# Performance work log

Hardware: AMD Instinct MI355X
Metric: run time of the kernel (lower is better)

## Reference

```python
import jax, jax.numpy as jnp
import numpy as np

B, N, D_IN, D, H_HEADS, DH, M_LAND, ITERS, NCLS = 2, 16384, 1024, 512, 8, 64, 256, 6, 2


def layer_norm(x, g, b, eps=1e-5):
    mu = x.mean(-1, keepdims=True)
    var = ((x - mu) ** 2).mean(-1, keepdims=True)
    return (x - mu) * jax.lax.rsqrt(var + eps) * g + b


def pinv_iter(x, iters):
    # Moore-Penrose pseudo-inverse via Newton-Schulz style iteration (lucidrains nystrom-attention)
    col = jnp.abs(x).sum(-1)
    row = jnp.abs(x).sum(-2)
    z = jnp.swapaxes(x, -1, -2) / (jnp.max(col) * jnp.max(row))
    I = jnp.eye(x.shape[-1], dtype=x.dtype)
    for _ in range(iters):
        xz = x @ z
        z = 0.25 * z @ (13.0 * I - xz @ (15.0 * I - xz @ (7.0 * I - xz)))
    return z


def depthwise_conv(x, w, pad_h, pad_w):
    # x: [B,C,H,W], w: [C,1,kh,kw], groups=C
    return jax.lax.conv_general_dilated(
        x, w, (1, 1), ((pad_h, pad_h), (pad_w, pad_w)),
        dimension_numbers=('NCHW', 'OIHW', 'NCHW'), feature_group_count=x.shape[1])


def nystrom_attention(x, w_qkv, w_out, b_out, res_w):
    b, n, _ = x.shape
    pad = (-n) % M_LAND
    xp = jnp.pad(x, ((0, 0), (pad, 0), (0, 0)))  # pad at front
    npad = n + pad
    qkv = xp @ w_qkv                              # [b, npad, 3D]
    q, k, v = jnp.split(qkv, 3, axis=-1)
    split_heads = lambda t: t.reshape(b, npad, H_HEADS, DH).transpose(0, 2, 1, 3)
    q = split_heads(q) * (DH ** -0.5)
    k = split_heads(k)
    v = split_heads(v)
    l = npad // M_LAND
    # landmarks: mean over contiguous groups '(m l) d -> m d'
    ql = q.reshape(b, H_HEADS, M_LAND, l, DH).mean(3)
    kl = k.reshape(b, H_HEADS, M_LAND, l, DH).mean(3)
    sim1 = jnp.einsum('bhnd,bhmd->bhnm', q, kl)   # [b,h,npad,m]
    sim2 = jnp.einsum('bhid,bhjd->bhij', ql, kl)  # [b,h,m,m]
    sim3 = jnp.einsum('bhmd,bhnd->bhmn', ql, k)   # [b,h,m,npad]
    a1 = jax.nn.softmax(sim1, -1)
    a2 = jax.nn.softmax(sim2, -1)
    a3 = jax.nn.softmax(sim3, -1)
    a2inv = pinv_iter(a2, ITERS)
    out = (a1 @ a2inv) @ (a3 @ v)                 # [b,h,npad,dh]
    # residual depthwise conv over sequence dim, kernel (33,1), per head
    out = out + depthwise_conv(v, res_w, 16, 0)
    out = out.transpose(0, 2, 1, 3).reshape(b, npad, D)
    out = out @ w_out + b_out                     # dropout is identity in eval
    return out[:, -n:]


def ppeg(x, Hs, Ws, w7, b7, w5, b5, w3, b3):
    Bx, _, C = x.shape
    cls_tok, feat = x[:, :1], x[:, 1:]
    f = feat.transpose(0, 2, 1).reshape(Bx, C, Hs, Ws)
    y = (f
         + depthwise_conv(f, w7, 3, 3) + b7[None, :, None, None]
         + depthwise_conv(f, w5, 2, 2) + b5[None, :, None, None]
         + depthwise_conv(f, w3, 1, 1) + b3[None, :, None, None])
    y = y.reshape(Bx, C, Hs * Ws).transpose(0, 2, 1)
    return jnp.concatenate([cls_tok, y], axis=1)


def _forward(x, w_feat, b_feat, cls_token, ln1_g, ln1_b, qkv1, out1_w, out1_b, res1_w,
             ppeg_w7, ppeg_b7, ppeg_w5, ppeg_b5, ppeg_w3, ppeg_b3,
             ln2_g, ln2_b, qkv2, out2_w, out2_b, res2_w, lnf_g, lnf_b, cls_w, cls_b):
    h = jax.nn.gelu(x @ w_feat + b_feat)          # feature embed (dropout off)
    n = h.shape[1]
    side = int(np.ceil(np.sqrt(n)))
    add = side * side - n
    h = jnp.concatenate([h, h[:, :add]], axis=1)  # pad bag to square
    cls = jnp.broadcast_to(cls_token, (h.shape[0], 1, D))
    h = jnp.concatenate([cls, h], axis=1)
    h = h + nystrom_attention(layer_norm(h, ln1_g, ln1_b), qkv1, out1_w, out1_b, res1_w)
    h = ppeg(h, side, side, ppeg_w7, ppeg_b7, ppeg_w5, ppeg_b5, ppeg_w3, ppeg_b3)
    h = h + nystrom_attention(layer_norm(h, ln2_g, ln2_b), qkv2, out2_w, out2_b, res2_w)
    feat0 = layer_norm(h, lnf_g, lnf_b)[:, 0]
    return feat0 @ cls_w + cls_b                  # logits [B, n_classes]


def setup_inputs() -> dict:
    key = jax.random.key(0)
    ks = jax.random.split(key, 16)
    s = jnp.float32(0.02)
    return {
        'x': jax.random.normal(ks[0], (B, N, D_IN), jnp.float32),
        'w_feat': jax.random.normal(ks[1], (D_IN, D), jnp.float32) * s,
        'b_feat': jnp.zeros((D,), jnp.float32),
        'cls_token': jax.random.normal(ks[2], (1, 1, D), jnp.float32) * jnp.float32(1e-6),
        'ln1_g': jnp.ones((D,), jnp.float32), 'ln1_b': jnp.zeros((D,), jnp.float32),
        'qkv1': jax.random.normal(ks[3], (D, 3 * D), jnp.float32) * s,
        'out1_w': jax.random.normal(ks[4], (D, D), jnp.float32) * s,
        'out1_b': jnp.zeros((D,), jnp.float32),
        'res1_w': jax.random.normal(ks[5], (H_HEADS, 1, 33, 1), jnp.float32) * s,
        'ppeg_w7': jax.random.normal(ks[6], (D, 1, 7, 7), jnp.float32) * s,
        'ppeg_b7': jnp.zeros((D,), jnp.float32),
        'ppeg_w5': jax.random.normal(ks[7], (D, 1, 5, 5), jnp.float32) * s,
        'ppeg_b5': jnp.zeros((D,), jnp.float32),
        'ppeg_w3': jax.random.normal(ks[8], (D, 1, 3, 3), jnp.float32) * s,
        'ppeg_b3': jnp.zeros((D,), jnp.float32),
        'ln2_g': jnp.ones((D,), jnp.float32), 'ln2_b': jnp.zeros((D,), jnp.float32),
        'qkv2': jax.random.normal(ks[9], (D, 3 * D), jnp.float32) * s,
        'out2_w': jax.random.normal(ks[10], (D, D), jnp.float32) * s,
        'out2_b': jnp.zeros((D,), jnp.float32),
        'res2_w': jax.random.normal(ks[11], (H_HEADS, 1, 33, 1), jnp.float32) * s,
        'lnf_g': jnp.ones((D,), jnp.float32), 'lnf_b': jnp.zeros((D,), jnp.float32),
        'cls_w': jax.random.normal(ks[12], (D, NCLS), jnp.float32) * s,
        'cls_b': jnp.zeros((NCLS,), jnp.float32),
    }


def reference(x, w_feat, b_feat, cls_token, ln1_g, ln1_b, qkv1, out1_w, out1_b, res1_w,
              ppeg_w7, ppeg_b7, ppeg_w5, ppeg_b5, ppeg_w3, ppeg_b3,
              ln2_g, ln2_b, qkv2, out2_w, out2_b, res2_w, lnf_g, lnf_b, cls_w, cls_b):
    return _forward(x, w_feat, b_feat, cls_token, ln1_g, ln1_b, qkv1, out1_w, out1_b, res1_w,
                    ppeg_w7, ppeg_b7, ppeg_w5, ppeg_b5, ppeg_w3, ppeg_b3,
                    ln2_g, ln2_b, qkv2, out2_w, out2_b, res2_w, lnf_g, lnf_b, cls_w, cls_b)
```

## Files before the change

kernel.cpp:

```cpp
#include <hip/hip_runtime.h>
#include <cstdint>
#include <cstddef>

#define BB 2
#define TT 16385
#define NPAD 16640
#define DD 512
#define HH 8
#define DHH 64
#define MLAND 256
#define PADF 255
#define A3KC 26
#define A3CH 640

typedef __attribute__((ext_vector_type(8))) _Float16 f16x8;
typedef __attribute__((ext_vector_type(4))) float f32x4;

__device__ __forceinline__ float gelu_f(float v) {
  float c = 0.7978845608028654f * (v + 0.044715f * v * v * v);
  return 0.5f * v * (1.0f + tanhf(c));
}

__device__ __forceinline__ unsigned short f16_1(float a) {
  _Float16 h = (_Float16)a;
  return __builtin_bit_cast(unsigned short, h);
}
__device__ __forceinline__ float f16f(unsigned u) {
  return (float)__builtin_bit_cast(_Float16, (unsigned short)(u & 0xffffu));
}
__device__ __forceinline__ unsigned pk_f16(float a, float b) {
  return (unsigned)f16_1(a) | ((unsigned)f16_1(b) << 16);
}
__device__ __forceinline__ void split2h(float a, float b, unsigned& hi, unsigned& lo) {
  _Float16 ah = (_Float16)a, bh = (_Float16)b;
  hi = (unsigned)__builtin_bit_cast(unsigned short, ah) |
       ((unsigned)__builtin_bit_cast(unsigned short, bh) << 16);
  lo = pk_f16(a - (float)ah, b - (float)bh);
}
__device__ __forceinline__ void store4h(float4 v, unsigned short* dh,
                                        unsigned short* dl) {
  unsigned h0, l0, h1, l1;
  split2h(v.x, v.y, h0, l0);
  split2h(v.z, v.w, h1, l1);
  *(uint2*)dh = make_uint2(h0, h1);
  *(uint2*)dl = make_uint2(l0, l1);
}

__global__ void k_set_cls(float* __restrict__ h, const float* __restrict__ cls) {
  h[(size_t)blockIdx.x * TT * DD + threadIdx.x] = cls[threadIdx.x];
}
__global__ void k_copy_cls(float* __restrict__ dst, const float* __restrict__ src) {
  size_t o = (size_t)blockIdx.x * TT * DD + threadIdx.x;
  dst[o] = src[o];
}

__global__ __launch_bounds__(256) void k_cvt_wt(
    const float* __restrict__ W, unsigned short* __restrict__ Wth, int K, int N) {
  __shared__ float tile[32][33];
  int kb = blockIdx.x * 32, nb = blockIdx.y * 32;
  int t = threadIdx.x;
  int tr = t >> 3, tc4 = (t & 7) * 4;
  float4 v = *(const float4*)(W + (size_t)(kb + tr) * N + nb + tc4);
  tile[tr][tc4 + 0] = v.x;
  tile[tr][tc4 + 1] = v.y;
  tile[tr][tc4 + 2] = v.z;
  tile[tr][tc4 + 3] = v.w;
  __syncthreads();
  int n = nb + tr;
  ushort4 hs;
  hs.x = f16_1(tile[tc4 + 0][tr]);
  hs.y = f16_1(tile[tc4 + 1][tr]);
  hs.z = f16_1(tile[tc4 + 2][tr]);
  hs.w = f16_1(tile[tc4 + 3][tr]);
  *(ushort4*)(Wth + (size_t)n * K + kb + tc4) = hs;
}

template <int MODE>
__global__ __launch_bounds__(512) void k_gemm_mfma(
    const float* __restrict__ A, const unsigned short* __restrict__ Aph,
    const unsigned short* __restrict__ Apl, const unsigned short* __restrict__ Wth,
    const float* __restrict__ bias, void* __restrict__ Cv, int M, int K, int N,
    int lda) {
  __shared__ short Ash[128][44];
  __shared__ short Asl[128][44];
  __shared__ short Bsh[256][44];
  const int t = threadIdx.x;
  int nRow = gridDim.x, nCol = gridDim.y;
  int lin = blockIdx.x + blockIdx.y * nRow;
  int chunk = 8 * nCol;
  int group = lin / chunk;
  int rem = lin - group * chunk;
  int gbase = group * 8;
  int Geff = nRow - gbase;
  if (Geff > 8) Geff = 8;
  const int rb = (gbase + rem % Geff) * 128;
  const int cb = (rem / Geff) * 256;
  const float* Ab = A;
  float* Cf = (float*)Cv;
  unsigned short* Ch = (unsigned short*)Cv;
  if (MODE == 2) {
    int b = blockIdx.z;
    Ab = A + (size_t)b * NPAD * DD + (size_t)PADF * DD;
    Cf = (float*)Cv + (size_t)b * TT * DD;
  }
  const int lane = t & 63, wv = t >> 6;
  const int wr = wv >> 2, wc = wv & 3;
  const int fr = lane & 15, kg = lane >> 4;
  const int srow = t >> 2, skh = (t & 3) * 8;
  const int brow = t >> 1, bkh = (t & 1) * 16;

  f32x4 acc[4][4];
  f32x4 zero4 = {0.f, 0.f, 0.f, 0.f};
#pragma unroll
  for (int i = 0; i < 4; ++i)
#pragma unroll
    for (int j = 0; j < 4; ++j) acc[i][j] = zero4;

  for (int k0 = 0; k0 < K; k0 += 32) {
    __syncthreads();
    if (MODE == 1) {
      const unsigned short* ph = Aph + (size_t)(rb + srow) * lda + k0 + skh;
      const unsigned short* pl = Apl + (size_t)(rb + srow) * lda + k0 + skh;
      *(uint4*)&Ash[srow][skh] = *(const uint4*)ph;
      *(uint4*)&Asl[srow][skh] = *(const uint4*)pl;
    } else {
      int grow = rb + srow;
      float4 f0 = {0, 0, 0, 0}, f1 = {0, 0, 0, 0};
      if (grow < M) {
        const float* p = Ab + (size_t)grow * lda + k0 + skh;
        f0 = *(const float4*)p;
        f1 = *(const float4*)(p + 4);
      }
      unsigned h0, h1, h2, h3, l0, l1, l2, l3;
      split2h(f0.x, f0.y, h0, l0);
      split2h(f0.z, f0.w, h1, l1);
      split2h(f1.x, f1.y, h2, l2);
      split2h(f1.z, f1.w, h3, l3);
      *(uint4*)&Ash[srow][skh] = make_uint4(h0, h1, h2, h3);
      *(uint4*)&Asl[srow][skh] = make_uint4(l0, l1, l2, l3);
    }
    {
      const unsigned short* ph = Wth + (size_t)(cb + brow) * K + k0 + bkh;
      *(uint4*)&Bsh[brow][bkh] = *(const uint4*)ph;
      *(uint4*)&Bsh[brow][bkh + 8] = *(const uint4*)(ph + 8);
    }
    __syncthreads();
    f16x8 ah[4], al[4];
#pragma unroll
    for (int mf = 0; mf < 4; ++mf) {
      ah[mf] = *(const f16x8*)&Ash[wr * 64 + mf * 16 + fr][kg * 8];
      al[mf] = *(const f16x8*)&Asl[wr * 64 + mf * 16 + fr][kg * 8];
    }
#pragma unroll
    for (int nf = 0; nf < 4; ++nf) {
      f16x8 bhf = *(const f16x8*)&Bsh[wc * 64 + nf * 16 + fr][kg * 8];
#pragma unroll
      for (int mf = 0; mf < 4; ++mf) {
        acc[mf][nf] =
            __builtin_amdgcn_mfma_f32_16x16x32_f16(ah[mf], bhf, acc[mf][nf], 0, 0, 0);
        acc[mf][nf] =
            __builtin_amdgcn_mfma_f32_16x16x32_f16(al[mf], bhf, acc[mf][nf], 0, 0, 0);
      }
    }
  }
#pragma unroll
  for (int mf = 0; mf < 4; ++mf) {
#pragma unroll
    for (int r = 0; r < 4; ++r) {
      int row = rb + wr * 64 + mf * 16 + kg * 4 + r;
      if (MODE == 2 && row >= M) continue;
      size_t orow = (MODE == 0) ? (size_t)(row + (row >> 14) + 1) : (size_t)row;
#pragma unroll
      for (int nf = 0; nf < 4; ++nf) {
        int col = cb + wc * 64 + nf * 16 + fr;
        float v = acc[mf][nf][r];
        if (MODE == 0) {
          Cf[orow * DD + col] = gelu_f(v + bias[col]);
        } else if (MODE == 1) {
          Ch[orow * (size_t)N + col] = f16_1(v);
        } else {
          float old = Cf[orow * DD + col];
          Cf[orow * DD + col] = old + v + bias[col];
        }
      }
    }
  }
}

__global__ __launch_bounds__(256) void k_ln_pad(
    unsigned short* __restrict__ xph, unsigned short* __restrict__ xpl,
    const float* __restrict__ h, const float* __restrict__ gam,
    const float* __restrict__ bet) {
  int w = threadIdx.x >> 6, lane = threadIdx.x & 63;
  int row = blockIdx.x * 4 + w;
  if (row >= BB * TT) return;
  int b = row / TT, i = row - b * TT;
  const float* src = h + (size_t)row * DD;
  float4 x0 = *(const float4*)(src + lane * 4);
  float4 x1 = *(const float4*)(src + 256 + lane * 4);
  float s = x0.x + x0.y + x0.z + x0.w + x1.x + x1.y + x1.z + x1.w;
  for (int o = 32; o; o >>= 1) s += __shfl_xor(s, o);
  float mu = s * (1.f / 512.f);
  float q = (x0.x - mu) * (x0.x - mu) + (x0.y - mu) * (x0.y - mu) +
            (x0.z - mu) * (x0.z - mu) + (x0.w - mu) * (x0.w - mu) +
            (x1.x - mu) * (x1.x - mu) + (x1.y - mu) * (x1.y - mu) +
            (x1.z - mu) * (x1.z - mu) + (x1.w - mu) * (x1.w - mu);
  for (int o = 32; o; o >>= 1) q += __shfl_xor(q, o);
  float rs = rsqrtf(q * (1.f / 512.f) + 1e-5f);
  float4 g0 = *(const float4*)(gam + lane * 4);
  float4 g1 = *(const float4*)(gam + 256 + lane * 4);
  float4 b0 = *(const float4*)(bet + lane * 4);
  float4 b1 = *(const float4*)(bet + 256 + lane * 4);
  float4 o0, o1;
  o0.x = (x0.x - mu) * rs * g0.x + b0.x;
  o0.y = (x0.y - mu) * rs * g0.y + b0.y;
  o0.z = (x0.z - mu) * rs * g0.z + b0.z;
  o0.w = (x0.w - mu) * rs * g0.w + b0.w;
  o1.x = (x1.x - mu) * rs * g1.x + b1.x;
  o1.y = (x1.y - mu) * rs * g1.y + b1.y;
  o1.z = (x1.z - mu) * rs * g1.z + b1.z;
  o1.w = (x1.w - mu) * rs * g1.w + b1.w;
  size_t ro = ((size_t)b * NPAD + PADF + i) * DD;
  store4h(o0, xph + ro + lane * 4, xpl + ro + lane * 4);
  store4h(o1, xph + ro + 256 + lane * 4, xpl + ro + 256 + lane * 4);
}

__global__ void k_zero_pad(unsigned short* __restrict__ xph,
                           unsigned short* __restrict__ xpl) {
  int r = blockIdx.x;
  int b = r / PADF, j = r - b * PADF;
  size_t ro = ((size_t)b * NPAD + j) * DD;
  ((unsigned*)(xph + ro))[threadIdx.x] = 0u;
  ((unsigned*)(xpl + ro))[threadIdx.x] = 0u;
}

__global__ __launch_bounds__(256) void k_landmarks(
    float* __restrict__ ql, float* __restrict__ kl,
    const unsigned short* __restrict__ qkv) {
  int t = threadIdx.x;
  int mi = t >> 6, d = t & 63;
  int blk = blockIdx.x;
  int bh = blk >> 6, mg = blk & 63;
  int b = bh >> 3, h = bh & 7;
  int m = mg * 4 + mi;
  const unsigned short* base = qkv + (size_t)b * NPAD * 1536 + h * 64 + d;
  float sq = 0.f, sk = 0.f;
  int t0 = m * 65;
  for (int j = 0; j < 65; ++j) {
    const unsigned short* p = base + (size_t)(t0 + j) * 1536;
    sq += f16f(p[0]);
    sk += f16f(p[512]);
  }
  ql[((size_t)bh * 256 + m) * 64 + d] = sq * (0.125f / 65.f);
  kl[((size_t)bh * 256 + m) * 64 + d] = sk * (1.f / 65.f);
}

__global__ __launch_bounds__(256) void k_sim2(
    float* __restrict__ sim, const float* __restrict__ ql, const float* __restrict__ kl) {
  __shared__ __align__(16) float Aq[64][68];
  __shared__ __align__(16) float Bk[64][68];
  int t = threadIdx.x;
  int tj = blockIdx.x, ti = blockIdx.y, bh = blockIdx.z;
  int r = t >> 2, cc = (t & 3) * 16;
  const float* ap = ql + ((size_t)bh * 256 + ti * 64 + r) * 64 + cc;
  const float* bp = kl + ((size_t)bh * 256 + tj * 64 + r) * 64 + cc;
#pragma unroll
  for (int i = 0; i < 16; i += 4) {
    *(float4*)&Aq[r][cc + i] = *(const float4*)(ap + i);
    *(float4*)&Bk[r][cc + i] = *(const float4*)(bp + i);
  }
  __syncthreads();
  int tx = t & 15, ty = t >> 4;
  float acc[4][4];
#pragma unroll
  for (int i = 0; i < 4; ++i)
#pragma unroll
    for (int j = 0; j < 4; ++j) acc[i][j] = 0.f;
  for (int d = 0; d < 64; d += 4) {
    float4 a4[4], b4[4];
#pragma unroll
    for (int ii = 0; ii < 4; ++ii) a4[ii] = *(float4*)&Aq[ty * 4 + ii][d];
#pragma unroll
    for (int jj = 0; jj < 4; ++jj) b4[jj] = *(float4*)&Bk[tx * 4 + jj][d];
#pragma unroll
    for (int ii = 0; ii < 4; ++ii)
#pragma unroll
      for (int jj = 0; jj < 4; ++jj)
        acc[ii][jj] += a4[ii].x * b4[jj].x + a4[ii].y * b4[jj].y + a4[ii].z * b4[jj].z +
                       a4[ii].w * b4[jj].w;
  }
#pragma unroll
  for (int ii = 0; ii < 4; ++ii)
#pragma unroll
    for (int jj = 0; jj < 4; ++jj)
      sim[((size_t)bh * 256 + ti * 64 + ty * 4 + ii) * 256 + tj * 64 + tx * 4 + jj] =
          acc[ii][jj];
}

__global__ __launch_bounds__(256) void k_softmax256(float* __restrict__ a) {
  int w = threadIdx.x >> 6, lane = threadIdx.x & 63;
  size_t row = (size_t)blockIdx.x * 4 + w;
  float* p = a + row * 256 + lane * 4;
  float4 v = *(float4*)p;
  float m = fmaxf(fmaxf(v.x, v.y), fmaxf(v.z, v.w));
  for (int o = 32; o; o >>= 1) m = fmaxf(m, __shfl_xor(m, o));
  v.x = expf(v.x - m); v.y = expf(v.y - m);
  v.z = expf(v.z - m); v.w = expf(v.w - m);
  float s = v.x + v.y + v.z + v.w;
  for (int o = 32; o; o >>= 1) s += __shfl_xor(s, o);
  float inv = 1.f / s;
  v.x *= inv; v.y *= inv; v.z *= inv; v.w *= inv;
  *(float4*)p = v;
}

__global__ void k_pinv_sums(float* __restrict__ red, const float* __restrict__ a2) {
  int bh = blockIdx.x, t = threadIdx.x;
  const float* Ab = a2 + (size_t)bh * 65536;
  float s = 0.f;
  for (int i = 0; i < 256; ++i) s += fabsf(Ab[(size_t)i * 256 + t]);
  red[bh * 256 + t] = s;
  float c = 0.f;
  const float* rp = Ab + (size_t)t * 256;
  for (int j = 0; j < 256; j += 4) {
    float4 v = *(const float4*)(rp + j);
    c += fabsf(v.x) + fabsf(v.y) + fabsf(v.z) + fabsf(v.w);
  }
  red[4096 + bh * 256 + t] = c;
}

__global__ void k_pinv_scale(float* __restrict__ red) {
  __shared__ float sm[8];
  int t = threadIdx.x;
  float m1 = 0.f, m2 = 0.f;
  for (int k = t; k < 4096; k += 256) {
    m1 = fmaxf(m1, red[k]);
    m2 = fmaxf(m2, red[4096 + k]);
  }
  for (int o = 32; o; o >>= 1) {
    m1 = fmaxf(m1, __shfl_xor(m1, o));
    m2 = fmaxf(m2, __shfl_xor(m2, o));
  }
  int w = t >> 6;
  if ((t & 63) == 0) { sm[w] = m1; sm[4 + w] = m2; }
  __syncthreads();
  if (t == 0) {
    float a = fmaxf(fmaxf(sm[0], sm[1]), fmaxf(sm[2], sm[3]));
    float b = fmaxf(fmaxf(sm[4], sm[5]), fmaxf(sm[6], sm[7]));
    red[8192] = 1.0f / (a * b);
  }
}

__global__ void k_zinit(float* __restrict__ z, const float* __restrict__ a2,
                        const float* __restrict__ red) {
  float s = red[8192];
  int i = blockIdx.x, bh = blockIdx.y, j = threadIdx.x;
  z[((size_t)bh * 256 + i) * 256 + j] = a2[((size_t)bh * 256 + j) * 256 + i] * s;
}

__device__ __forceinline__ void bmm_core(
    short (*Ash)[136], short (*Asl)[136], short (*Bsh)[136], short (*Bsl)[136],
    const float* __restrict__ Ab, const float* __restrict__ Bb, int i0, int j0, int N,
    int t, f32x4 (&acc)[4]) {
  const int lane = t & 63, w = t >> 6;
  const int fr = lane & 15, kg = lane >> 4;
  const int ar = t >> 2, akseg = (t & 3) * 32;
  for (int k0 = 0; k0 < 256; k0 += 128) {
    __syncthreads();
    {
      const float* p = Ab + (size_t)(i0 + ar) * 256 + k0 + akseg;
#pragma unroll
      for (int q = 0; q < 4; ++q) {
        float4 f0 = *(const float4*)(p + q * 8);
        float4 f1 = *(const float4*)(p + q * 8 + 4);
        unsigned h0, h1, h2, h3, l0, l1, l2, l3;
        split2h(f0.x, f0.y, h0, l0);
        split2h(f0.z, f0.w, h1, l1);
        split2h(f1.x, f1.y, h2, l2);
        split2h(f1.z, f1.w, h3, l3);
        *(uint4*)&Ash[ar][akseg + q * 8] = make_uint4(h0, h1, h2, h3);
        *(uint4*)&Asl[ar][akseg + q * 8] = make_uint4(l0, l1, l2, l3);
      }
    }
    {
#pragma unroll
      for (int pass = 0; pass < 8; ++pass) {
        int kr = pass * 16 + (t >> 4);
        int jseg = (t & 15) * 4;
        const float* p = Bb + (size_t)(k0 + kr) * N + j0 + jseg;
        float4 f = *(const float4*)p;
        float fv[4] = {f.x, f.y, f.z, f.w};
#pragma unroll
        for (int c = 0; c < 4; ++c) {
          _Float16 hh = (_Float16)fv[c];
          float lo = fv[c] - (float)hh;
          Bsh[jseg + c][kr] = (short)__builtin_bit_cast(unsigned short, hh);
          Bsl[jseg + c][kr] = (short)f16_1(lo);
        }
      }
    }
    __syncthreads();
#pragma unroll
    for (int kw = 0; kw < 4; ++kw) {
      f16x8 bhf = *(const f16x8*)&Bsh[w * 16 + fr][kw * 32 + kg * 8];
      f16x8 blf = *(const f16x8*)&Bsl[w * 16 + fr][kw * 32 + kg * 8];
#pragma unroll
      for (int mf = 0; mf < 4; ++mf) {
        f16x8 ah = *(const f16x8*)&Ash[mf * 16 + fr][kw * 32 + kg * 8];
        f16x8 al = *(const f16x8*)&Asl[mf * 16 + fr][kw * 32 + kg * 8];
        acc[mf] = __builtin_amdgcn_mfma_f32_16x16x32_f16(ah, bhf, acc[mf], 0, 0, 0);
        acc[mf] = __builtin_amdgcn_mfma_f32_16x16x32_f16(al, bhf, acc[mf], 0, 0, 0);
        acc[mf] = __builtin_amdgcn_mfma_f32_16x16x32_f16(ah, blf, acc[mf], 0, 0, 0);
      }
    }
  }
}

__global__ __launch_bounds__(256) void k_bmm_poly(
    const float* __restrict__ A, const float* __restrict__ Bm,
    const float* __restrict__ E, float* __restrict__ C, float a1, float d1, float e1,
    int N) {
  __shared__ short Ash[64][136];
  __shared__ short Asl[64][136];
  __shared__ short Bsh[64][136];
  __shared__ short Bsl[64][136];
  const int t = threadIdx.x;
  const int bh = blockIdx.z;
  const int i0 = blockIdx.y * 64, j0 = blockIdx.x * 64;
  const int lane = t & 63, w = t >> 6;
  const int fr = lane & 15, kg = lane >> 4;
  f32x4 acc[4];
  f32x4 zero4 = {0.f, 0.f, 0.f, 0.f};
#pragma unroll
  for (int i = 0; i < 4; ++i) acc[i] = zero4;
  bmm_core(Ash, Asl, Bsh, Bsl, A + (size_t)bh * 65536, Bm + (size_t)bh * 256 * N, i0,
           j0, N, t, acc);
  int j = j0 + w * 16 + fr;
#pragma unroll
  for (int mf = 0; mf < 4; ++mf) {
#pragma unroll
    for (int rr = 0; rr < 4; ++rr) {
      int i = i0 + mf * 16 + kg * 4 + rr;
      float v = acc[mf][rr];
      size_t off = (size_t)bh * 256 * N + (size_t)i * N + j;
      float out = a1 * v + ((i == j) ? d1 : 0.f);
      if (E) out += e1 * E[off];
      C[off] = out;
    }
  }
}

__global__ __launch_bounds__(256) void k_bmm_dual(
    const float* __restrict__ A0, const float* __restrict__ A1,
    const float* __restrict__ Bm, float* __restrict__ C0, float* __restrict__ C1,
    float s) {
  __shared__ short Ash[64][136];
  __shared__ short Asl[64][136];
  __shared__ short Bsh[64][136];
  __shared__ short Bsl[64][136];
  const int t = threadIdx.x;
  const int z = blockIdx.z;
  const int bh = z & 15;
  const int sel = z >> 4;
  const float* A = sel ? A1 : A0;
  float* C = sel ? C1 : C0;
  const int i0 = blockIdx.y * 64, j0 = blockIdx.x * 64;
  const int lane = t & 63, w = t >> 6;
  const int fr = lane & 15, kg = lane >> 4;
  f32x4 acc[4];
  f32x4 zero4 = {0.f, 0.f, 0.f, 0.f};
#pragma unroll
  for (int i = 0; i < 4; ++i) acc[i] = zero4;
  bmm_core(Ash, Asl, Bsh, Bsl, A + (size_t)bh * 65536, Bm + (size_t)bh * 65536, i0, j0,
           256, t, acc);
  int j = j0 + w * 16 + fr;
#pragma unroll
  for (int mf = 0; mf < 4; ++mf) {
#pragma unroll
    for (int rr = 0; rr < 4; ++rr) {
      int i = i0 + mf * 16 + kg * 4 + rr;
      size_t off = (size_t)bh * 65536 + (size_t)i * 256 + j;
      C[off] = s * acc[mf][rr];
    }
  }
}

__global__ __launch_bounds__(256, 2) void k_a3v_mfma(
    float* __restrict__ pacc, float* __restrict__ pL,
    const float* __restrict__ ql, const unsigned short* __restrict__ qkv) {
  __shared__ short Ks[64][72];
  __shared__ short Vt[64][72];
  __shared__ short Ps[4][64][72];
  const int t = threadIdx.x;
  const int bh = blockIdx.x;
  const int kc = blockIdx.y;
  const int b = bh >> 3, h = bh & 7;
  const int lane = t & 63, w = t >> 6;
  const int fr = lane & 15, kg = lane >> 4;

  f16x8 qf[4][2];
#pragma unroll
  for (int nf = 0; nf < 4; ++nf) {
    const float* qp = ql + ((size_t)bh * 256 + w * 64 + nf * 16 + fr) * 64 + kg * 8;
#pragma unroll
    for (int kw = 0; kw < 2; ++kw) {
      float4 a = *(const float4*)(qp + kw * 32);
      float4 c = *(const float4*)(qp + kw * 32 + 4);
      uint4 uu = make_uint4(pk_f16(a.x, a.y), pk_f16(a.z, a.w), pk_f16(c.x, c.y),
                            pk_f16(c.z, c.w));
      qf[nf][kw] = *(f16x8*)&uu;
    }
  }
  f32x4 oacc[4][4];
  f32x4 zero4 = {0.f, 0.f, 0.f, 0.f};
#pragma unroll
  for (int i = 0; i < 4; ++i)
#pragma unroll
    for (int j = 0; j < 4; ++j) oacc[i][j] = zero4;
  float Lp[4] = {0.f, 0.f, 0.f, 0.f};

  const int skey = t >> 2, sd = (t & 3) * 16;
  const unsigned short* kbase = qkv + (size_t)b * NPAD * 1536 + 512 + h * 64 + sd;

  for (int it = 0; it < A3CH / 64; ++it) {
    int nt = kc * A3CH + it * 64;
    __syncthreads();
    {
      const unsigned short* kp = kbase + (size_t)(nt + skey) * 1536;
      *(uint4*)&Ks[skey][sd] = *(const uint4*)kp;
      *(uint4*)&Ks[skey][sd + 8] = *(const uint4*)(kp + 8);
      const unsigned short* vp = kp + 512;
      uint4 v01 = *(const uint4*)vp;
      uint4 v23 = *(const uint4*)(vp + 8);
      Vt[sd + 0][skey] = (short)v01.x;
      Vt[sd + 1][skey] = (short)(v01.x >> 16);
      Vt[sd + 2][skey] = (short)v01.y;
      Vt[sd + 3][skey] = (short)(v01.y >> 16);
      Vt[sd + 4][skey] = (short)v01.z;
      Vt[sd + 5][skey] = (short)(v01.z >> 16);
      Vt[sd + 6][skey] = (short)v01.w;
      Vt[sd + 7][skey] = (short)(v01.w >> 16);
      Vt[sd + 8][skey] = (short)v23.x;
      Vt[sd + 9][skey] = (short)(v23.x >> 16);
      Vt[sd + 10][skey] = (short)v23.y;
      Vt[sd + 11][skey] = (short)(v23.y >> 16);
      Vt[sd + 12][skey] = (short)v23.z;
      Vt[sd + 13][skey] = (short)(v23.z >> 16);
      Vt[sd + 14][skey] = (short)v23.w;
      Vt[sd + 15][skey] = (short)(v23.w >> 16);
    }
    __syncthreads();
    f32x4 sacc[4][4];
#pragma unroll
    for (int i = 0; i < 4; ++i)
#pragma unroll
      for (int j = 0; j < 4; ++j) sacc[i][j] = zero4;
#pragma unroll
    for (int kw = 0; kw < 2; ++kw) {
      f16x8 kf[4];
#pragma unroll
      for (int mf = 0; mf < 4; ++mf)
        kf[mf] = *(const f16x8*)&Ks[mf * 16 + fr][kw * 32 + kg * 8];
#pragma unroll
      for (int mf = 0; mf < 4; ++mf)
#pragma unroll
        for (int nf = 0; nf < 4; ++nf)
          sacc[mf][nf] = __builtin_amdgcn_mfma_f32_16x16x32_f16(kf[mf], qf[nf][kw],
                                                                sacc[mf][nf], 0, 0, 0);
    }
#pragma unroll
    for (int mf = 0; mf < 4; ++mf)
#pragma unroll
      for (int nf = 0; nf < 4; ++nf) {
        f32x4 s = sacc[mf][nf];
        float p0 = __expf(s[0]);
        float p1 = __expf(s[1]);
        float p2 = __expf(s[2]);
        float p3 = __expf(s[3]);
        Lp[nf] += (p0 + p1) + (p2 + p3);
        uint2 pw = make_uint2(pk_f16(p0, p1), pk_f16(p2, p3));
        *(uint2*)&Ps[w][nf * 16 + fr][mf * 16 + kg * 4] = pw;
      }
    __syncthreads();
#pragma unroll
    for (int kw = 0; kw < 2; ++kw) {
      f16x8 vf[4], pf[4];
#pragma unroll
      for (int mf = 0; mf < 4; ++mf)
        vf[mf] = *(const f16x8*)&Vt[mf * 16 + fr][kw * 32 + kg * 8];
#pragma unroll
      for (int nf = 0; nf < 4; ++nf)
        pf[nf] = *(const f16x8*)&Ps[w][nf * 16 + fr][kw * 32 + kg * 8];
#pragma unroll
      for (int mf = 0; mf < 4; ++mf)
#pragma unroll
        for (int nf = 0; nf < 4; ++nf)
          oacc[mf][nf] = __builtin_amdgcn_mfma_f32_16x16x32_f16(vf[mf], pf[nf],
                                                                oacc[mf][nf], 0, 0, 0);
    }
  }
  size_t obase = ((size_t)kc * 16 + bh) * 256;
#pragma unroll
  for (int mf = 0; mf < 4; ++mf)
#pragma unroll
    for (int nf = 0; nf < 4; ++nf) {
      int lm = w * 64 + nf * 16 + fr;
      *(f32x4*)(pacc + (obase + lm) * 64 + mf * 16 + kg * 4) = oacc[mf][nf];
    }
#pragma unroll
  for (int nf = 0; nf < 4; ++nf) {
    Lp[nf] += __shfl_xor(Lp[nf], 16);
    Lp[nf] += __shfl_xor(Lp[nf], 32);
  }
  if (lane < 16) {
#pragma unroll
    for (int nf = 0; nf < 4; ++nf)
      pL[obase + w * 64 + nf * 16 + lane] = Lp[nf];
  }
}

__global__ __launch_bounds__(64) void k_a3v_red(
    float* __restrict__ bv, const float* __restrict__ pacc,
    const float* __restrict__ pL) {
  int row = blockIdx.x;
  int d = threadIdx.x;
  float A = 0.f, L = 0.f;
#pragma unroll
  for (int c = 0; c < A3KC; ++c) {
    size_t pr = (size_t)c * 4096 + row;
    A += pacc[pr * 64 + d];
    L += pL[pr];
  }
  bv[(size_t)row * 64 + d] = A / L;
}

__global__ __launch_bounds__(256, 2) void k_att1(
    float* __restrict__ attout, const unsigned short* __restrict__ qkv,
    const float* __restrict__ kl, const float* __restrict__ w2) {
  __shared__ short KLs[64][72];
  __shared__ short W2t[64][72];
  __shared__ short Ps[4][64][72];
  const int t = threadIdx.x;
  const int tile = blockIdx.x, bh = blockIdx.y;
  const int b = bh >> 3, h = bh & 7;
  const int lane = t & 63, w = t >> 6;
  const int fr = lane & 15, kg = lane >> 4;
  const int n0 = tile * 256;

  f16x8 qf[4][2];
#pragma unroll
  for (int nf = 0; nf < 4; ++nf) {
    const unsigned short* qp =
        qkv + ((size_t)b * NPAD + n0 + w * 64 + nf * 16 + fr) * 1536 + h * 64 + kg * 8;
    qf[nf][0] = *(const f16x8*)qp;
    qf[nf][1] = *(const f16x8*)(qp + 32);
  }
  f32x4 oacc[4][4];
  f32x4 zero4 = {0.f, 0.f, 0.f, 0.f};
#pragma unroll
  for (int i = 0; i < 4; ++i)
#pragma unroll
    for (int j = 0; j < 4; ++j) oacc[i][j] = zero4;
  float Lp[4] = {0.f, 0.f, 0.f, 0.f};

  const int sr = t >> 2, sc = (t & 3) * 16;
  for (int cb = 0; cb < 4; ++cb) {
    __syncthreads();
    {
      const float* kp = kl + ((size_t)bh * 256 + cb * 64 + sr) * 64 + sc;
      float4 k0 = *(const float4*)kp;
      float4 k1 = *(const float4*)(kp + 4);
      float4 k2 = *(const float4*)(kp + 8);
      float4 k3 = *(const float4*)(kp + 12);
      *(uint4*)&KLs[sr][sc] =
          make_uint4(pk_f16(k0.x * 0.125f, k0.y * 0.125f),
                     pk_f16(k0.z * 0.125f, k0.w * 0.125f),
                     pk_f16(k1.x * 0.125f, k1.y * 0.125f),
                     pk_f16(k1.z * 0.125f, k1.w * 0.125f));
      *(uint4*)&KLs[sr][sc + 8] =
          make_uint4(pk_f16(k2.x * 0.125f, k2.y * 0.125f),
                     pk_f16(k2.z * 0.125f, k2.w * 0.125f),
                     pk_f16(k3.x * 0.125f, k3.y * 0.125f),
                     pk_f16(k3.z * 0.125f, k3.w * 0.125f));
      const float* wp = w2 + ((size_t)bh * 256 + cb * 64 + sr) * 64 + sc;
      float4 v0 = *(const float4*)wp;
      float4 v1 = *(const float4*)(wp + 4);
      float4 v2 = *(const float4*)(wp + 8);
      float4 v3 = *(const float4*)(wp + 12);
      W2t[sc + 0][sr] = (short)f16_1(v0.x);
      W2t[sc + 1][sr] = (short)f16_1(v0.y);
      W2t[sc + 2][sr] = (short)f16_1(v0.z);
      W2t[sc + 3][sr] = (short)f16_1(v0.w);
      W2t[sc + 4][sr] = (short)f16_1(v1.x);
      W2t[sc + 5][sr] = (short)f16_1(v1.y);
      W2t[sc + 6][sr] = (short)f16_1(v1.z);
      W2t[sc + 7][sr] = (short)f16_1(v1.w);
      W2t[sc + 8][sr] = (short)f16_1(v2.x);
      W2t[sc + 9][sr] = (short)f16_1(v2.y);
      W2t[sc + 10][sr] = (short)f16_1(v2.z);
      W2t[sc + 11][sr] = (short)f16_1(v2.w);
      W2t[sc + 12][sr] = (short)f16_1(v3.x);
      W2t[sc + 13][sr] = (short)f16_1(v3.y);
      W2t[sc + 14][sr] = (short)f16_1(v3.z);
      W2t[sc + 15][sr] = (short)f16_1(v3.w);
    }
    __syncthreads();
    f32x4 sacc[4][4];
#pragma unroll
    for (int i = 0; i < 4; ++i)
#pragma unroll
      for (int j = 0; j < 4; ++j) sacc[i][j] = zero4;
#pragma unroll
    for (int kw = 0; kw < 2; ++kw) {
      f16x8 kf[4];
#pragma unroll
      for (int mf = 0; mf < 4; ++mf)
        kf[mf] = *(const f16x8*)&KLs[mf * 16 + fr][kw * 32 + kg * 8];
#pragma unroll
      for (int mf = 0; mf < 4; ++mf)
#pragma unroll
        for (int nf = 0; nf < 4; ++nf)
          sacc[mf][nf] = __builtin_amdgcn_mfma_f32_16x16x32_f16(kf[mf], qf[nf][kw],
                                                                sacc[mf][nf], 0, 0, 0);
    }
#pragma unroll
    for (int mf = 0; mf < 4; ++mf)
#pragma unroll
      for (int nf = 0; nf < 4; ++nf) {
        f32x4 s = sacc[mf][nf];
        float p0 = __expf(s[0]);
        float p1 = __expf(s[1]);
        float p2 = __expf(s[2]);
        float p3 = __expf(s[3]);
        Lp[nf] += (p0 + p1) + (p2 + p3);
        uint2 pw = make_uint2(pk_f16(p0, p1), pk_f16(p2, p3));
        *(uint2*)&Ps[w][nf * 16 + fr][mf * 16 + kg * 4] = pw;
      }
    __syncthreads();
#pragma unroll
    for (int kw = 0; kw < 2; ++kw) {
      f16x8 vf[4], pf[4];
#pragma unroll
      for (int mf = 0; mf < 4; ++mf)
        vf[mf] = *(const f16x8*)&W2t[mf * 16 + fr][kw * 32 + kg * 8];
#pragma unroll
      for (int nf = 0; nf < 4; ++nf)
        pf[nf] = *(const f16x8*)&Ps[w][nf * 16 + fr][kw * 32 + kg * 8];
#pragma unroll
      for (int mf = 0; mf < 4; ++mf)
#pragma unroll
        for (int nf = 0; nf < 4; ++nf)
          oacc[mf][nf] = __builtin_amdgcn_mfma_f32_16x16x32_f16(vf[mf], pf[nf],
                                                                oacc[mf][nf], 0, 0, 0);
    }
  }
#pragma unroll
  for (int nf = 0; nf < 4; ++nf) {
    Lp[nf] += __shfl_xor(Lp[nf], 16);
    Lp[nf] += __shfl_xor(Lp[nf], 32);
  }
#pragma unroll
  for (int nf = 0; nf < 4; ++nf) {
    float inv = 1.0f / Lp[nf];
    int tok = n0 + w * 64 + nf * 16 + fr;
#pragma unroll
    for (int mf = 0; mf < 4; ++mf) {
      f32x4 o = oacc[mf][nf];
      o[0] *= inv; o[1] *= inv; o[2] *= inv; o[3] *= inv;
      *(f32x4*)(attout + ((size_t)b * NPAD + tok) * DD + h * 64 + mf * 16 + kg * 4) = o;
    }
  }
}

__global__ __launch_bounds__(256) void k_convres(
    float* __restrict__ attout, const unsigned short* __restrict__ qkv,
    const float* __restrict__ resw) {
  __shared__ float vS[96][68];
  __shared__ float w33[33];
  int t = threadIdx.x;
  int tb = blockIdx.x, bh = blockIdx.y;
  int b = bh >> 3, h = bh & 7;
  int n0 = tb * 64;
  if (t < 33) w33[t] = resw[h * 33 + t];
  int sc = (t & 3) * 16;
#pragma unroll
  for (int pass = 0; pass < 2; ++pass) {
    int r = (t >> 2) + pass * 64;
    if (r < 96) {
      int seq = n0 - 16 + r;
      if (seq >= 0 && seq < NPAD) {
        const unsigned short* p =
            qkv + ((size_t)b * NPAD + seq) * 1536 + 1024 + h * 64 + sc;
        uint4 u0 = *(const uint4*)p;
        uint4 u1 = *(const uint4*)(p + 8);
        vS[r][sc + 0] = f16f(u0.x); vS[r][sc + 1] = f16f(u0.x >> 16);
        vS[r][sc + 2] = f16f(u0.y); vS[r][sc + 3] = f16f(u0.y >> 16);
        vS[r][sc + 4] = f16f(u0.z); vS[r][sc + 5] = f16f(u0.z >> 16);
        vS[r][sc + 6] = f16f(u0.w); vS[r][sc + 7] = f16f(u0.w >> 16);
        vS[r][sc + 8] = f16f(u1.x); vS[r][sc + 9] = f16f(u1.x >> 16);
        vS[r][sc + 10] = f16f(u1.y); vS[r][sc + 11] = f16f(u1.y >> 16);
        vS[r][sc + 12] = f16f(u1.z); vS[r][sc + 13] = f16f(u1.z >> 16);
        vS[r][sc + 14] = f16f(u1.w); vS[r][sc + 15] = f16f(u1.w >> 16);
      } else {
#pragma unroll
        for (int i = 0; i < 16; ++i) vS[r][sc + i] = 0.f;
      }
    }
  }
  __syncthreads();
  int tg = t >> 5;
  int d2 = (t & 31) * 2;
#pragma unroll
  for (int tk = 0; tk < 8; ++tk) {
    int tokL = tg * 8 + tk;
    float ax = 0.f, ay = 0.f;
    for (int k = 0; k < 33; ++k) {
      float2 v = *(float2*)&vS[tokL + k][d2];
      ax += w33[k] * v.x;
      ay += w33[k] * v.y;
    }
    float* dst = attout + ((size_t)b * NPAD + n0 + tokL) * DD + h * 64 + d2;
    float2 o = *(float2*)dst;
    o.x += ax;
    o.y += ay;
    *(float2*)dst = o;
  }
}

__global__ __launch_bounds__(128) void k_ppeg(
    float* __restrict__ hB, const float* __restrict__ hA,
    const float* __restrict__ w7, const float* __restrict__ b7,
    const float* __restrict__ w5, const float* __restrict__ b5,
    const float* __restrict__ w3, const float* __restrict__ b3) {
  __shared__ float cw[49][128];
  int t = threadIdx.x;
  int i = blockIdx.x >> 2;
  int j0 = (blockIdx.x & 3) * 32;
  int cg = blockIdx.y, b = blockIdx.z;
  int c = cg * 128 + t;
#pragma unroll
  for (int k = 0; k < 49; ++k) cw[k][t] = w7[c * 49 + k];
#pragma unroll
  for (int di = 0; di < 5; ++di)
#pragma unroll
    for (int dj = 0; dj < 5; ++dj)
      cw[(di + 1) * 7 + dj + 1][t] += w5[c * 25 + di * 5 + dj];
#pragma unroll
  for (int di = 0; di < 3; ++di)
#pragma unroll
    for (int dj = 0; dj < 3; ++dj)
      cw[(di + 2) * 7 + dj + 2][t] += w3[c * 9 + di * 3 + dj];
  cw[24][t] += 1.0f;
  float bias = b7[c] + b5[c] + b3[c];
  const float* base = hA + (size_t)b * TT * DD + DD + c;
  float* obase = hB + (size_t)b * TT * DD + DD + c;
  float acc[32];
#pragma unroll
  for (int j = 0; j < 32; ++j) acc[j] = bias;
  for (int di = 0; di < 7; ++di) {
    int ii = i + di - 3;
    if ((unsigned)ii >= 128u) continue;
    float win[38];
#pragma unroll
    for (int w = 0; w < 38; ++w) {
      int col = j0 - 3 + w;
      win[w] = ((unsigned)col < 128u) ? base[(size_t)(ii * 128 + col) * DD] : 0.f;
    }
#pragma unroll
    for (int dj = 0; dj < 7; ++dj) {
      float wv = cw[di * 7 + dj][t];
#pragma unroll
      for (int j = 0; j < 32; ++j) acc[j] += win[j + dj] * wv;
    }
  }
#pragma unroll
  for (int j = 0; j < 32; ++j) obase[(size_t)(i * 128 + j0 + j) * DD] = acc[j];
}

__global__ __launch_bounds__(512) void k_final(
    float* __restrict__ out, const float* __restrict__ h,
    const float* __restrict__ g, const float* __restrict__ be,
    const float* __restrict__ cw, const float* __restrict__ cbias) {
  __shared__ float sm[16];
  int t = threadIdx.x;
  for (int b = 0; b < 2; ++b) {
    const float* row = h + (size_t)b * TT * DD;
    float x = row[t];
    float s = x;
    for (int o = 32; o; o >>= 1) s += __shfl_xor(s, o);
    if ((t & 63) == 0) sm[t >> 6] = s;
    __syncthreads();
    float mu = 0.f;
    for (int i = 0; i < 8; ++i) mu += sm[i];
    mu *= (1.f / 512.f);
    __syncthreads();
    float d = x - mu;
    s = d * d;
    for (int o = 32; o; o >>= 1) s += __shfl_xor(s, o);
    if ((t & 63) == 0) sm[t >> 6] = s;
    __syncthreads();
    float var = 0.f;
    for (int i = 0; i < 8; ++i) var += sm[i];
    var *= (1.f / 512.f);
    float rs = rsqrtf(var + 1e-5f);
    __syncthreads();
    float f = d * rs * g[t] + be[t];
    float p0 = f * cw[2 * t], p1 = f * cw[2 * t + 1];
    for (int o = 32; o; o >>= 1) {
      p0 += __shfl_xor(p0, o);
      p1 += __shfl_xor(p1, o);
    }
    if ((t & 63) == 0) {
      sm[t >> 6] = p0;
      sm[8 + (t >> 6)] = p1;
    }
    __syncthreads();
    if (t == 0) {
      float q0 = 0.f, q1 = 0.f;
      for (int i = 0; i < 8; ++i) {
        q0 += sm[i];
        q1 += sm[8 + i];
      }
      out[b * 2 + 0] = q0 + cbias[0];
      out[b * 2 + 1] = q1 + cbias[1];
    }
    __syncthreads();
  }
}

static void run_attn(float* h, const float* lng, const float* lnb,
                     const float* wqkv, const float* wout, const float* bout,
                     const float* resw, float* xp, unsigned short* qkvh, float* ql,
                     float* kl, float* a2, float* z0, float* z1, float* xz, float* xz2,
                     float* yB, float* yC, float* bv, float* w2, float* red,
                     float* Sbuf, unsigned short* wth, hipStream_t stream) {
  unsigned short* xph = (unsigned short*)xp;
  unsigned short* xpl = xph + (size_t)BB * NPAD * DD;
  k_zero_pad<<<BB * PADF, 256, 0, stream>>>(xph, xpl);
  k_ln_pad<<<(BB * TT + 3) / 4, 256, 0, stream>>>(xph, xpl, h, lng, lnb);
  k_cvt_wt<<<dim3(DD / 32, 1536 / 32), 256, 0, stream>>>(wqkv, wth, DD, 1536);
  k_gemm_mfma<1><<<dim3(BB * NPAD / 128, 1536 / 256), 512, 0, stream>>>(
      nullptr, xph, xpl, wth, nullptr, qkvh, BB * NPAD, DD, 1536, DD);
  k_landmarks<<<1024, 256, 0, stream>>>(ql, kl, qkvh);
  float* pacc = Sbuf;
  float* pL = Sbuf + (size_t)A3KC * 4096 * 64;
  k_a3v_mfma<<<dim3(16, A3KC), 256, 0, stream>>>(pacc, pL, ql, qkvh);
  k_a3v_red<<<4096, 64, 0, stream>>>(bv, pacc, pL);
  k_sim2<<<dim3(4, 4, 16), 256, 0, stream>>>(a2, ql, kl);
  k_softmax256<<<1024, 256, 0, stream>>>(a2);
  k_pinv_sums<<<16, 256, 0, stream>>>(red, a2);
  k_pinv_scale<<<1, 256, 0, stream>>>(red);
  k_zinit<<<dim3(256, 16), 256, 0, stream>>>(z0, a2, red);
  float* zc = z0;
  float* zn = z1;
  float* P = xz;
  float* Pn = xz2;
  k_bmm_poly<<<dim3(4, 4, 16), 256, 0, stream>>>(a2, zc, nullptr, P, 1.f, 0.f, 0.f, 256);
  for (int it = 0; it < 6; ++it) {
    k_bmm_poly<<<dim3(4, 4, 16), 256, 0, stream>>>(P, P, P, yB, 1.f, 15.f, -7.f, 256);
    k_bmm_poly<<<dim3(4, 4, 16), 256, 0, stream>>>(P, yB, nullptr, yC, -1.f, 13.f, 0.f, 256);
    k_bmm_dual<<<dim3(4, 4, 32), 256, 0, stream>>>(zc, P, yC, zn, Pn, 0.25f);
    float* tmp = zc; zc = zn; zn = tmp;
    tmp = P; P = Pn; Pn = tmp;
  }
  k_bmm_poly<<<dim3(1, 4, 16), 256, 0, stream>>>(zc, bv, nullptr, w2, 1.f, 0.f, 0.f, 64);
  k_att1<<<dim3(NPAD / 256, 16), 256, 0, stream>>>(xp, qkvh, kl, w2);
  k_convres<<<dim3(NPAD / 64, 16), 256, 0, stream>>>(xp, qkvh, resw);
  k_cvt_wt<<<dim3(DD / 32, DD / 32), 256, 0, stream>>>(wout, wth, DD, DD);
  k_gemm_mfma<2><<<dim3(129, 2, BB), 512, 0, stream>>>(xp, nullptr, nullptr, wth, bout,
                                                       h, TT, DD, DD, DD);
}

extern "C" void kernel_launch(void* const* d_in, const int* in_sizes, int n_in,
                              void* d_out, int out_size, void* d_ws, size_t ws_size,
                              hipStream_t stream) {
  const float* x        = (const float*)d_in[0];
  const float* w_feat   = (const float*)d_in[1];
  const float* b_feat   = (const float*)d_in[2];
  const float* cls_tok  = (const float*)d_in[3];
  const float* ln1_g    = (const float*)d_in[4];
  const float* ln1_b    = (const float*)d_in[5];
  const float* qkv1     = (const float*)d_in[6];
  const float* out1_w   = (const float*)d_in[7];
  const float* out1_b   = (const float*)d_in[8];
  const float* res1_w   = (const float*)d_in[9];
  const float* ppeg_w7  = (const float*)d_in[10];
  const float* ppeg_b7  = (const float*)d_in[11];
  const float* ppeg_w5  = (const float*)d_in[12];
  const float* ppeg_b5  = (const float*)d_in[13];
  const float* ppeg_w3  = (const float*)d_in[14];
  const float* ppeg_b3  = (const float*)d_in[15];
  const float* ln2_g    = (const float*)d_in[16];
  const float* ln2_b    = (const float*)d_in[17];
  const float* qkv2     = (const float*)d_in[18];
  const float* out2_w   = (const float*)d_in[19];
  const float* out2_b   = (const float*)d_in[20];
  const float* res2_w   = (const float*)d_in[21];
  const float* lnf_g    = (const float*)d_in[22];
  const float* lnf_b    = (const float*)d_in[23];
  const float* cls_w    = (const float*)d_in[24];
  const float* cls_b    = (const float*)d_in[25];

  float* ws = (float*)d_ws;
  size_t off = 0;
  float* hA  = ws + off; off += (size_t)BB * TT * DD;
  float* hB  = ws + off; off += (size_t)BB * TT * DD;
  float* xp  = ws + off; off += (size_t)BB * NPAD * DD;
  float* qkvf = ws + off; off += (size_t)BB * NPAD * 3 * DD;
  unsigned short* qkvh = (unsigned short*)qkvf;
  float* ql  = ws + off; off += (size_t)BB * HH * 256 * 64;
  float* kl  = ws + off; off += (size_t)BB * HH * 256 * 64;
  float* a2  = ws + off; off += (size_t)16 * 65536;
  float* z0  = ws + off; off += (size_t)16 * 65536;
  float* z1  = ws + off; off += (size_t)16 * 65536;
  float* xz  = ws + off; off += (size_t)16 * 65536;
  float* xz2 = ws + off; off += (size_t)16 * 65536;
  float* yB  = ws + off; off += (size_t)16 * 65536;
  float* yC  = ws + off; off += (size_t)16 * 65536;
  float* bv  = ws + off; off += (size_t)BB * HH * 256 * 64;
  float* w2  = ws + off; off += (size_t)BB * HH * 256 * 64;
  float* red = ws + off; off += 8448;
  unsigned short* wth = (unsigned short*)(ws + off); off += 393216;

  k_set_cls<<<2, 512, 0, stream>>>(hA, cls_tok);
  k_cvt_wt<<<dim3(1024 / 32, DD / 32), 256, 0, stream>>>(w_feat, wth, 1024, DD);
  k_gemm_mfma<0><<<dim3(32768 / 128, DD / 256), 512, 0, stream>>>(
      x, nullptr, nullptr, wth, b_feat, hA, 32768, 1024, DD, 1024);
  run_attn(hA, ln1_g, ln1_b, qkv1, out1_w, out1_b, res1_w, xp, qkvh, ql, kl, a2, z0, z1,
           xz, xz2, yB, yC, bv, w2, red, hB, wth, stream);
  k_copy_cls<<<2, 512, 0, stream>>>(hB, hA);
  k_ppeg<<<dim3(512, 4, 2), 128, 0, stream>>>(hB, hA, ppeg_w7, ppeg_b7, ppeg_w5, ppeg_b5,
                                              ppeg_w3, ppeg_b3);
  run_attn(hB, ln2_g, ln2_b, qkv2, out2_w, out2_b, res2_w, xp, qkvh, ql, kl, a2, z0, z1,
           xz, xz2, yB, yC, bv, w2, red, hA, wth, stream);
  k_final<<<1, 512, 0, stream>>>((float*)d_out, hB, lnf_g, lnf_b, cls_w, cls_b);
}
```

Before: 1.622 ms.

## Add specialized QKV GEMM with async global-to-LDS loads and double buffering

Replaces the generic MFMA GEMM for the QKV projection with a dedicated kernel. It streams A (hi/lo f16 split) and W tiles straight into LDS through global_load_lds, uses a swizzled layout, double-buffers across the K loop with explicit vmcnt waits, and maps blocks in grouped rasterization order for L2 reuse. The goal is to hide global-memory latency and cut register staging in this GEMM. It relies on hand-placed waitcnt and barrier ordering, which could be fragile.

After: 1.606 ms. Within noise of the previous version (-1.0%).

```diff
diff --git a/kernel.cpp b/kernel.cpp
--- a/kernel.cpp
+++ b/kernel.cpp
@@ -44,6 +44,12 @@
   split2h(v.z, v.w, h1, l1);
   *(uint2*)dh = make_uint2(h0, h1);
   *(uint2*)dl = make_uint2(l0, l1);
+}
+
+__device__ __forceinline__ void gload16(const unsigned short* g, short* l) {
+  __builtin_amdgcn_global_load_lds(
+      (const __attribute__((address_space(1))) void*)g,
+      (__attribute__((address_space(3))) void*)l, 16, 0, 0);
 }
 
 __global__ void k_set_cls(float* __restrict__ h, const float* __restrict__ cls) {
@@ -182,6 +188,100 @@
           float old = Cf[orow * DD + col];
           Cf[orow * DD + col] = old + v + bias[col];
         }
+      }
+    }
+  }
+}
+
+__global__ __launch_bounds__(512) void k_gemm_qkv8(
+    const unsigned short* __restrict__ Aph, const unsigned short* __restrict__ Apl,
+    const unsigned short* __restrict__ Wth, unsigned short* __restrict__ Ch) {
+  __shared__ __align__(16) short Ah[2][128][64];
+  __shared__ __align__(16) short Al[2][128][64];
+  __shared__ __align__(16) short Bs[2][256][64];
+  const int t = threadIdx.x;
+  int nRow = gridDim.x, nCol = gridDim.y;
+  int lin = blockIdx.x + blockIdx.y * nRow;
+  int chunk = 8 * nCol;
+  int group = lin / chunk;
+  int rem = lin - group * chunk;
+  int gbase = group * 8;
+  int Geff = nRow - gbase;
+  if (Geff > 8) Geff = 8;
+  const int rb = (gbase + rem % Geff) * 128;
+  const int cb = (rem / Geff) * 256;
+  const int lane = t & 63, wv = t >> 6;
+  const int wr = wv >> 2, wc = wv & 3;
+  const int fr = lane & 15, kg = lane >> 4;
+  const int lr8 = lane >> 3;
+  const int ss = (lane & 7) ^ lr8;
+
+  f32x4 acc[4][4];
+  f32x4 zero4 = {0.f, 0.f, 0.f, 0.f};
+#pragma unroll
+  for (int i = 0; i < 4; ++i)
+#pragma unroll
+    for (int j = 0; j < 4; ++j) acc[i][j] = zero4;
+
+  auto STAGE = [&](int kt, int bf) {
+    const int k0 = kt * 64;
+#pragma unroll
+    for (int j = 0; j < 2; ++j) {
+      int lr = wv * 16 + j * 8;
+      gload16(Aph + (size_t)(rb + lr + lr8) * DD + k0 + ss * 8, &Ah[bf][lr][0]);
+      gload16(Apl + (size_t)(rb + lr + lr8) * DD + k0 + ss * 8, &Al[bf][lr][0]);
+    }
+#pragma unroll
+    for (int j = 0; j < 4; ++j) {
+      int lr = wv * 32 + j * 8;
+      gload16(Wth + (size_t)(cb + lr + lr8) * DD + k0 + ss * 8, &Bs[bf][lr][0]);
+    }
+  };
+
+  STAGE(0, 0);
+  STAGE(1, 1);
+  for (int kt = 0; kt < 8; ++kt) {
+    if (kt < 7) {
+      asm volatile("s_waitcnt vmcnt(8)" ::: "memory");
+    } else {
+      asm volatile("s_waitcnt vmcnt(0)" ::: "memory");
+    }
+    __builtin_amdgcn_sched_barrier(0);
+    __builtin_amdgcn_s_barrier();
+    const int bf = kt & 1;
+#pragma unroll
+    for (int kw = 0; kw < 2; ++kw) {
+      const int sl = ((kw * 4 + kg) ^ (fr & 7)) * 8;
+      f16x8 ah[4], al[4];
+#pragma unroll
+      for (int mf = 0; mf < 4; ++mf) {
+        ah[mf] = *(const f16x8*)&Ah[bf][wr * 64 + mf * 16 + fr][sl];
+        al[mf] = *(const f16x8*)&Al[bf][wr * 64 + mf * 16 + fr][sl];
+      }
+#pragma unroll
+      for (int nf = 0; nf < 4; ++nf) {
+        f16x8 bhf = *(const f16x8*)&Bs[bf][wc * 64 + nf * 16 + fr][sl];
+#pragma unroll
+        for (int mf = 0; mf < 4; ++mf) {
+          acc[mf][nf] =
+              __builtin_amdgcn_mfma_f32_16x16x32_f16(ah[mf], bhf, acc[mf][nf], 0, 0, 0);
+          acc[mf][nf] =
+              __builtin_amdgcn_mfma_f32_16x16x32_f16(al[mf], bhf, acc[mf][nf], 0, 0, 0);
+        }
+      }
+    }
+    __builtin_amdgcn_s_barrier();
+    if (kt + 2 < 8) STAGE(kt + 2, bf);
+  }
+#pragma unroll
+  for (int mf = 0; mf < 4; ++mf) {
+#pragma unroll
+    for (int r = 0; r < 4; ++r) {
+      int row = rb + wr * 64 + mf * 16 + kg * 4 + r;
+#pragma unroll
+      for (int nf = 0; nf < 4; ++nf) {
+        int col = cb + wc * 64 + nf * 16 + fr;
+        Ch[(size_t)row * 1536 + col] = f16_1(acc[mf][nf][r]);
       }
     }
   }
@@ -938,8 +1038,8 @@
   k_zero_pad<<<BB * PADF, 256, 0, stream>>>(xph, xpl);
   k_ln_pad<<<(BB * TT + 3) / 4, 256, 0, stream>>>(xph, xpl, h, lng, lnb);
   k_cvt_wt<<<dim3(DD / 32, 1536 / 32), 256, 0, stream>>>(wqkv, wth, DD, 1536);
-  k_gemm_mfma<1><<<dim3(BB * NPAD / 128, 1536 / 256), 512, 0, stream>>>(
-      nullptr, xph, xpl, wth, nullptr, qkvh, BB * NPAD, DD, 1536, DD);
+  k_gemm_qkv8<<<dim3(BB * NPAD / 128, 1536 / 256), 512, 0, stream>>>(xph, xpl, wth,
+                                                                     qkvh);
   k_landmarks<<<1024, 256, 0, stream>>>(ql, kl, qkvh);
   float* pacc = Sbuf;
   float* pL = Sbuf + (size_t)A3KC * 4096 * 64;
```
